# Optimization experiments

Measured on AMD Instinct MI355X. Metric: run time of the kernel, lower is better.

The kernel has to match this reference:

```python
import jax, jax.numpy as jnp
import numpy as np

N_E = 1024      # codes per sub-codebook
E_DIM = 64      # code dimension
BETA = 0.25     # commitment cost (VectorQuantizer(n_e, e_dim, 0.25))


def setup_inputs() -> dict:
    key = jax.random.key(0)
    k1, k2 = jax.random.split(key)
    bs, c, h, w = 16, 512, 32, 32
    m = c // E_DIM  # 8 sub-codebooks
    z = jax.random.normal(k1, (bs, c, h, w), dtype=jnp.float32)
    # taming-style init: uniform(-1/n_e, 1/n_e)
    codebooks = jax.random.uniform(
        k2, (m, N_E, E_DIM), dtype=jnp.float32,
        minval=-1.0 / N_E, maxval=1.0 / N_E)
    return {"z": z, "codebooks": codebooks}


def reference(z, codebooks):
    bs, c, h, w = z.shape
    m, n_e, e_dim = codebooks.shape
    N = bs * h * w
    # [bs,c,h,w] -> [bs,h,w,c] -> [m, N, e_dim]: batched over all m sub-codebooks at once
    zf = z.transpose(0, 2, 3, 1).reshape(N, m, e_dim).transpose(1, 0, 2)

    # squared L2 distances: ||z||^2 + ||e||^2 - 2 z.e   -> [m, N, n_e]
    d = ((zf ** 2).sum(-1, keepdims=True)
         + (codebooks ** 2).sum(-1)[:, None, :]
         - 2.0 * jnp.einsum('mnd,mkd->mnk', zf, codebooks))
    idx = jnp.argmin(d, axis=-1)  # [m, N]

    # gather nearest codes: [m, N, e_dim]
    zq = jnp.take_along_axis(codebooks, idx[:, :, None], axis=1)

    # per-sub-codebook VQ loss, summed over m (loss = sum(loss_list))
    codebook_loss = jnp.mean((jax.lax.stop_gradient(zq) - zf) ** 2, axis=(1, 2))
    commit_loss = jnp.mean((zq - jax.lax.stop_gradient(zf)) ** 2, axis=(1, 2))
    loss = jnp.sum(codebook_loss + BETA * commit_loss)

    # straight-through estimator
    zq_st = zf + jax.lax.stop_gradient(zq - zf)

    # reassemble: [m,N,d] -> [N,m*d] -> [bs,h,w,c] -> [bs,c,h,w]
    z_vq = zq_st.transpose(1, 0, 2).reshape(bs, h, w, c).transpose(0, 3, 1, 2)

    # concat of per-codebook index tensors along dim 0
    min_encoding_indices = idx.reshape(-1)  # [m*N]
    # per-code occupancy counts summed over the m codebooks -> [n_e]
    bin_count = jnp.zeros((n_e,), jnp.int32).at[min_encoding_indices].add(1)

    return z_vq, loss, min_encoding_indices, bin_count
```

## Files before the change

kernel.cpp:

```cpp
#include <hip/hip_runtime.h>
#include <cfloat>

#define BS 16
#define CC 512
#define HWD 1024
#define NN 16384
#define MM 8
#define NE 1024
#define ED 64

#define LOSS_OFF 8388608
#define IDX_OFF  8388609
#define BIN_OFF  8519681

#define TAU 4e-5f
#define UWIN 400u

#define WS_B     0
#define WS_IDX   32768
#define WS_CNT   557056
#define WS_LIST  557088
#define WS_OF    688160
#define WS_CAND  720928
#define WS_BMAT  3866656

typedef __attribute__((ext_vector_type(8))) short bf16x8;
typedef __attribute__((ext_vector_type(16))) float f32x16;

__device__ __forceinline__ unsigned short f2bf(float f) {
    unsigned int u = __float_as_uint(f);
    unsigned int r = (u + 0x7fffu + ((u >> 16) & 1u)) >> 16;
    return (unsigned short)r;
}
__device__ __forceinline__ float bf2f(unsigned short h) {
    return __uint_as_float(((unsigned int)h) << 16);
}
__device__ __forceinline__ unsigned umin_(unsigned a, unsigned b) { return a < b ? a : b; }
__device__ __forceinline__ unsigned umax_(unsigned a, unsigned b) { return a > b ? a : b; }
__device__ __forceinline__ unsigned umin3(unsigned a, unsigned b, unsigned c) {
    return umin_(umin_(a, b), c);
}

__device__ __forceinline__ float mul_rn(float a, float b) {
#pragma clang fp contract(off)
    return a * b;
}
__device__ __forceinline__ float add_rn(float a, float b) {
#pragma clang fp contract(off)
    return a + b;
}
__device__ __forceinline__ float sub_rn(float a, float b) {
#pragma clang fp contract(off)
    return a - b;
}

__device__ __forceinline__ float np_sumsq64(const float* x) {
    float r[8];
#pragma unroll
    for (int j = 0; j < 8; ++j) r[j] = mul_rn(x[j], x[j]);
#pragma unroll
    for (int i = 8; i < 64; i += 8) {
#pragma unroll
        for (int j = 0; j < 8; ++j) r[j] = add_rn(r[j], mul_rn(x[i + j], x[i + j]));
    }
    return add_rn(add_rn(add_rn(r[0], r[1]), add_rn(r[2], r[3])),
                  add_rn(add_rn(r[4], r[5]), add_rn(r[6], r[7])));
}

__device__ __forceinline__ float np_dot64(const float* zsh, const float4* cr4) {
    float v0 = 0.f, v1 = 0.f, v2 = 0.f, v3 = 0.f;
#pragma unroll
    for (int t = 0; t < 4; ++t) {
        float4 e0 = cr4[t * 4 + 0];
        float4 e1 = cr4[t * 4 + 1];
        float4 e2 = cr4[t * 4 + 2];
        float4 e3 = cr4[t * 4 + 3];
        const int d0 = 16 * t;
        v0 = add_rn(mul_rn(zsh[d0 + 0], e0.x),
             add_rn(mul_rn(zsh[d0 + 4], e1.x),
             add_rn(mul_rn(zsh[d0 + 8], e2.x),
             add_rn(mul_rn(zsh[d0 + 12], e3.x), v0))));
        v1 = add_rn(mul_rn(zsh[d0 + 1], e0.y),
             add_rn(mul_rn(zsh[d0 + 5], e1.y),
             add_rn(mul_rn(zsh[d0 + 9], e2.y),
             add_rn(mul_rn(zsh[d0 + 13], e3.y), v1))));
        v2 = add_rn(mul_rn(zsh[d0 + 2], e0.z),
             add_rn(mul_rn(zsh[d0 + 6], e1.z),
             add_rn(mul_rn(zsh[d0 + 10], e2.z),
             add_rn(mul_rn(zsh[d0 + 14], e3.z), v2))));
        v3 = add_rn(mul_rn(zsh[d0 + 3], e0.w),
             add_rn(mul_rn(zsh[d0 + 7], e1.w),
             add_rn(mul_rn(zsh[d0 + 11], e2.w),
             add_rn(mul_rn(zsh[d0 + 15], e3.w), v3))));
    }
    return add_rn(add_rn(v0, v1), add_rn(v2, v3));
}

__global__ __launch_bounds__(256) void prep_kernel(const float* __restrict__ cb,
                                                   float* __restrict__ Bhat,
                                                   uint4* __restrict__ Bmat,
                                                   float* __restrict__ out,
                                                   int* __restrict__ cnt) {
    const int tid = threadIdx.x;
    if (blockIdx.x < 32) {
        int i = blockIdx.x * 256 + tid;
        if (i == 0) { out[LOSS_OFF] = 0.0f; cnt[0] = 0; cnt[1] = 0; }
        if (i < NE) out[BIN_OFF + i] = 0.0f;
        const float4* r4 = (const float4*)(cb + (size_t)i * ED);
        float x[ED];
#pragma unroll
        for (int q = 0; q < 16; ++q) {
            float4 v = r4[q];
            x[q*4+0] = v.x; x[q*4+1] = v.y; x[q*4+2] = v.z; x[q*4+3] = v.w;
        }
        Bhat[i] = np_sumsq64(x);
        return;
    }
    int t = (blockIdx.x - 32) * 256 + tid;
    int lane = t & 63;
    int ct = (t >> 6) & 31;
    int rem = t >> 11;
    int c = rem % 9;
    int m = rem / 9;
    int h = lane >> 5;
    int k = ct * 32 + (lane & 31);

    unsigned short v[8];
#pragma unroll
    for (int j = 0; j < 8; ++j) v[j] = 0;

    if (c < 8) {
        int d0 = 16 * (c & 3) + 8 * h;
        const float* e = cb + ((size_t)m * NE + k) * ED + d0;
#pragma unroll
        for (int j = 0; j < 8; ++j) {
            float f = -2.0f * e[j];
            unsigned short hi = f2bf(f);
            v[j] = (c >= 4) ? f2bf(f - bf2f(hi)) : hi;
        }
    } else if (h == 0) {
        const float* e = cb + ((size_t)m * NE + k) * ED;
        float s = 0.f;
#pragma unroll
        for (int d = 0; d < ED; ++d) s += e[d] * e[d];
        v[0] = f2bf(s);
        v[1] = 0x3F80;
    }
    uint4 o;
    o.x = (unsigned)v[0] | ((unsigned)v[1] << 16);
    o.y = (unsigned)v[2] | ((unsigned)v[3] << 16);
    o.z = (unsigned)v[4] | ((unsigned)v[5] << 16);
    o.w = (unsigned)v[6] | ((unsigned)v[7] << 16);
    Bmat[t] = o;
}

__global__ __launch_bounds__(512, 4) void argmin_kernel(
        const float* __restrict__ z, const uint4* __restrict__ Bmat,
        int* __restrict__ idx_out, int* __restrict__ cnt,
        int* __restrict__ list, unsigned short* __restrict__ cand) {
    const int tid = threadIdx.x;
    const int m = blockIdx.y;
    const int row0 = blockIdx.x * 256;
    const int w = tid >> 6;
    const int l = tid & 63;
    const int h = l >> 5;
    const int r5 = l & 31;

    __shared__ uint4 ldsB[3][9 * 2 * 64];

    const int n_mine = row0 + w * 32 + r5;
    const int b = n_mine >> 10;
    const int hw = n_mine & (HWD - 1);
    const float* zbase = z + (((size_t)(b * CC + m * ED)) << 10) + hw;

    bf16x8 zh[4], zl[4];
#pragma unroll
    for (int i = 0; i < 4; ++i) {
        int o = 2 * i + h;
#pragma unroll
        for (int j = 0; j < 8; ++j) {
            float f = zbase[(size_t)(8 * o + j) << 10];
            unsigned short hb = f2bf(f);
            unsigned short lb = f2bf(f - bf2f(hb));
            zh[i][j] = (short)hb;
            zl[i][j] = (short)lb;
        }
    }
    bf16x8 ones12 = {0, 0, 0, 0, 0, 0, 0, 0};
    if (h == 0) { ones12[0] = (short)0x3F80; ones12[1] = (short)0x3F80; }

    unsigned rbm = 0xFFFFFFF0u, rsec = 0xFFFFFFFFu, rinfo = 0;
    int ccnt = 0;
    unsigned cq0 = 0, cq1 = 0, cq2 = 0;
    auto push = [&](unsigned id) {
        cq2 = (cq2 << 16) | (cq1 >> 16);
        cq1 = (cq1 << 16) | (cq0 >> 16);
        cq0 = (cq0 << 16) | (id & 0xFFFFu);
        ccnt++;
    };

    auto stage = [&](int g, int bufi) {
        for (int seg = w; seg < 18; seg += 8) {
            int c = seg >> 1, ct2 = seg & 1;
            const uint4* src = Bmat +
                ((size_t)((m * 9 + c) * 32 + (g * 2 + ct2)) << 6) + l;
            uint4* dst = &ldsB[bufi][(c * 2 + ct2) * 64];
            __builtin_amdgcn_global_load_lds(
                (const __attribute__((address_space(1))) unsigned int*)src,
                (__attribute__((address_space(3))) unsigned int*)dst, 16, 0, 0);
        }
    };

    auto process = [&](const f32x16& acc, unsigned tile) {
        unsigned u[16];
#pragma unroll
        for (int s = 0; s < 16; ++s)
            u[s] = (__float_as_uint(acc[s]) & 0xFFFFFFF0u) | (unsigned)s;
        unsigned b0 = umin_(u[0], u[1]),  s0 = umax_(u[0], u[1]);
        unsigned b1 = umin_(u[2], u[3]),  s1 = umax_(u[2], u[3]);
        unsigned b2 = umin_(u[4], u[5]),  s2 = umax_(u[4], u[5]);
        unsigned b3 = umin_(u[6], u[7]),  s3 = umax_(u[6], u[7]);
        unsigned b4 = umin_(u[8], u[9]),  s4 = umax_(u[8], u[9]);
        unsigned b5 = umin_(u[10], u[11]), s5 = umax_(u[10], u[11]);
        unsigned b6 = umin_(u[12], u[13]), s6 = umax_(u[12], u[13]);
        unsigned b7 = umin_(u[14], u[15]), s7 = umax_(u[14], u[15]);
        unsigned B0 = umin_(b0, b1), S0 = umin3(umax_(b0, b1), s0, s1);
        unsigned B1 = umin_(b2, b3), S1 = umin3(umax_(b2, b3), s2, s3);
        unsigned B2 = umin_(b4, b5), S2 = umin3(umax_(b4, b5), s4, s5);
        unsigned B3 = umin_(b6, b7), S3 = umin3(umax_(b6, b7), s6, s7);
        unsigned C0 = umin_(B0, B1), T0 = umin3(umax_(B0, B1), S0, S1);
        unsigned C1 = umin_(B2, B3), T1 = umin3(umax_(B2, B3), S2, S3);
        unsigned bt = umin_(C0, C1), st = umin3(umax_(C0, C1), T0, T1);

        unsigned oldrbm = rbm;
        bool take = bt < oldrbm;
        unsigned newrbm = take ? bt : oldrbm;
        unsigned limit = newrbm + UWIN;
        rsec = umin3(rsec, st, take ? oldrbm : bt);
        int sbt = (int)(bt & 15u);
        if (take) {
            if (bt + UWIN < oldrbm) ccnt = 0;
            push(tile * 32u + ((unsigned)sbt & 3u) +
                 8u * ((unsigned)sbt >> 2) + 4u * (unsigned)h);
            rinfo = (tile << 4) | (unsigned)sbt;
        }
        rbm = newrbm;
        unsigned gatev = take ? st : bt;
        if (gatev < limit) {
#pragma unroll
            for (int s = 0; s < 16; ++s) {
                if (u[s] < limit && !(take && s == sbt))
                    push(tile * 32u + ((unsigned)s & 3u) +
                         8u * ((unsigned)s >> 2) + 4u * (unsigned)h);
            }
        }
    };

    stage(0, 0);
    stage(1, 1);
    asm volatile("s_waitcnt vmcnt(2)" ::: "memory");
    __builtin_amdgcn_s_barrier();

    int bR = 0;
    for (int g = 0; g < 16; ++g) {
        int bW = bR + 2; if (bW >= 3) bW -= 3;
        if (g < 14) stage(g + 2, bW);
        const uint4* Bb = &ldsB[bR][0];

        f32x16 a0, a1;
#pragma unroll
        for (int s = 0; s < 16; ++s) { a0[s] = 0.0f; a1[s] = 0.0f; }
        bf16x8 sh0[4], sh1[4];
        __builtin_amdgcn_s_setprio(1);
#pragma unroll
        for (int c = 0; c < 4; ++c) {
            bf16x8 af0 = *(const bf16x8*)&Bb[(c * 2 + 0) * 64 + l];
            bf16x8 af1 = *(const bf16x8*)&Bb[(c * 2 + 1) * 64 + l];
            sh0[c] = af0; sh1[c] = af1;
            a0 = __builtin_amdgcn_mfma_f32_32x32x16_bf16(af0, zh[c], a0, 0, 0, 0);
            a1 = __builtin_amdgcn_mfma_f32_32x32x16_bf16(af1, zh[c], a1, 0, 0, 0);
        }
#pragma unroll
        for (int c = 4; c < 8; ++c) {
            bf16x8 af0 = *(const bf16x8*)&Bb[(c * 2 + 0) * 64 + l];
            bf16x8 af1 = *(const bf16x8*)&Bb[(c * 2 + 1) * 64 + l];
            a0 = __builtin_amdgcn_mfma_f32_32x32x16_bf16(af0, zh[c & 3], a0, 0, 0, 0);
            a1 = __builtin_amdgcn_mfma_f32_32x32x16_bf16(af1, zh[c & 3], a1, 0, 0, 0);
        }
#pragma unroll
        for (int c = 0; c < 4; ++c) {
            a0 = __builtin_amdgcn_mfma_f32_32x32x16_bf16(sh0[c], zl[c], a0, 0, 0, 0);
            a1 = __builtin_amdgcn_mfma_f32_32x32x16_bf16(sh1[c], zl[c], a1, 0, 0, 0);
        }
        {
            bf16x8 af0 = *(const bf16x8*)&Bb[(8 * 2 + 0) * 64 + l];
            bf16x8 af1 = *(const bf16x8*)&Bb[(8 * 2 + 1) * 64 + l];
            a0 = __builtin_amdgcn_mfma_f32_32x32x16_bf16(af0, ones12, a0, 0, 0, 0);
            a1 = __builtin_amdgcn_mfma_f32_32x32x16_bf16(af1, ones12, a1, 0, 0, 0);
        }
        __builtin_amdgcn_s_setprio(0);
        process(a0, (unsigned)(g * 2 + 0));
        process(a1, (unsigned)(g * 2 + 1));

        if (g < 14) {
            asm volatile("s_waitcnt vmcnt(2)" ::: "memory");
        } else if (g == 14) {
            asm volatile("s_waitcnt vmcnt(0)" ::: "memory");
        }
        if (g < 15) __builtin_amdgcn_s_barrier();
        bR = (bR == 2) ? 0 : bR + 1;
    }

    unsigned short* myslots = cand + ((size_t)(m * NN + n_mine) * 2 + h) * 6;
    if (ccnt) {
        unsigned* cp = (unsigned*)myslots;
        cp[0] = cq0; cp[1] = cq1; cp[2] = cq2;
    }

    int pcnt = __shfl_xor(ccnt, 32, 64);

    unsigned ss = rinfo & 15u, tile = rinfo >> 4;
    int k = (int)(tile * 32 + (ss & 3u) + 8u * (ss >> 2) + 4u * (unsigned)h);
    unsigned orbm = __shfl_xor(rbm, 32, 64);
    int ok = __shfl_xor(k, 32, 64);
    unsigned orsec = __shfl_xor(rsec, 32, 64);
    bool take = orbm < rbm;
    unsigned lose = take ? rbm : orbm;
    unsigned fb = take ? orbm : rbm;
    int fk = take ? ok : k;
    unsigned fs = umin3(rsec, orsec, lose);
    if (l < 32) {
        int mn = m * NN + n_mine;
        idx_out[mn] = fk;
        float margin = __uint_as_float(fs & 0xFFFFFFF0u) -
                       __uint_as_float(fb & 0xFFFFFFF0u);
        if (margin < TAU) {
            int p = atomicAdd(cnt, 1);
            if (p < 32768) {
                int c0 = ccnt > 6 ? 7 : ccnt;
                int c1 = pcnt > 6 ? 7 : pcnt;
                list[p] = mn | (c0 << 20) | (c1 << 24);
            }
        }
    }
}

__global__ __launch_bounds__(256) void cand_kernel(
        const float* __restrict__ z, const float* __restrict__ cb,
        const float* __restrict__ Bhat, int* __restrict__ cnt,
        const int* __restrict__ list, const unsigned short* __restrict__ cand,
        int* __restrict__ idx_out, int* __restrict__ oflist) {
    const int tid = threadIdx.x;
    const int lane = tid & 63;
    const int wv = tid >> 6;
    const int wid = (blockIdx.x * 256 + tid) >> 6;
    const int nw = gridDim.x * 4;
    const int total = cnt[0] < 32768 ? cnt[0] : 32768;

    __shared__ float zsh[4][ED];

    for (int r = wid; r < total; r += nw) {
        const int e = list[r];
        const int mn = e & 0xFFFFF;
        const int c0 = (e >> 20) & 15;
        const int c1 = (e >> 24) & 15;
        if (c0 == 7 || c1 == 7) {
            if (lane == 0) {
                int q = atomicAdd(cnt + 1, 1);
                if (q < 8192) oflist[q] = mn;
            }
            continue;
        }
        const int m = mn >> 14;
        const int n = mn & (NN - 1);
        const int b = n >> 10;
        const int hw = n & (HWD - 1);

        zsh[wv][lane] = z[(((size_t)(b * CC + m * ED + lane)) << 10) + hw];

        int kj = -1;
        if (lane < c0) kj = cand[(size_t)mn * 12 + lane];
        else if (lane >= 8 && lane < 8 + c1) kj = cand[(size_t)mn * 12 + 6 + (lane - 8)];

        float A = np_sumsq64(&zsh[wv][0]);

        float dref = FLT_MAX;
        if (kj >= 0) {
            const float4* cr4 = (const float4*)(cb + ((size_t)m * NE + kj) * ED);
            float C = np_dot64(&zsh[wv][0], cr4);
            dref = sub_rn(add_rn(A, Bhat[m * NE + kj]), mul_rn(2.0f, C));
        }
        int kk = (kj >= 0) ? kj : NE;
#pragma unroll
        for (int off = 32; off >= 1; off >>= 1) {
            float ov = __shfl_down(dref, off, 64);
            int oi = __shfl_down(kk, off, 64);
            if (ov < dref || (ov == dref && oi < kk)) { dref = ov; kk = oi; }
        }
        if (lane == 0) idx_out[mn] = kk;
    }
}

__global__ __launch_bounds__(256) void emul_kernel(
        const float* __restrict__ z, const float* __restrict__ cb,
        const float* __restrict__ Bhat, const int* __restrict__ cnt,
        const int* __restrict__ oflist, int* __restrict__ idx_out) {
    const int tid = threadIdx.x;
    const int lane = tid & 63;
    const int w = tid >> 6;
    const int total = cnt[1] < 8192 ? cnt[1] : 8192;

    __shared__ float zsh[ED];
    __shared__ float rbest[4];
    __shared__ int ridx[4];

    for (int r = blockIdx.x; r < total; r += gridDim.x) {
        const int mn = oflist[r];
        const int m = mn >> 14;
        const int n = mn & (NN - 1);
        const int b = n >> 10;
        const int hw = n & (HWD - 1);

        __syncthreads();
        if (tid < ED) {
            const float* zbase = z + (((size_t)(b * CC + m * ED)) << 10) + hw;
            zsh[tid] = zbase[(size_t)tid << 10];
        }
        __syncthreads();

        const float A = np_sumsq64(zsh);
        const float* cbm = cb + (size_t)m * NE * ED;
        const float* Bm = Bhat + m * NE;
        float best = FLT_MAX;
        int bidx = NE;
#pragma unroll
        for (int kk = 0; kk < 4; ++kk) {
            const int k = kk * 256 + tid;
            const float4* cr4 = (const float4*)(cbm + (size_t)k * ED);
            float C = np_dot64(zsh, cr4);
            float dk = sub_rn(add_rn(A, Bm[k]), mul_rn(2.0f, C));
            if (dk < best || (dk == best && k < bidx)) { best = dk; bidx = k; }
        }
#pragma unroll
        for (int off = 32; off >= 1; off >>= 1) {
            float ov = __shfl_down(best, off, 64);
            int oi = __shfl_down(bidx, off, 64);
            if (ov < best || (ov == best && oi < bidx)) { best = ov; bidx = oi; }
        }
        if (lane == 0) { rbest[w] = best; ridx[w] = bidx; }
        __syncthreads();
        if (tid == 0) {
            float bb = rbest[0]; int bi = ridx[0];
#pragma unroll
            for (int i = 1; i < 4; ++i) {
                if (rbest[i] < bb || (rbest[i] == bb && ridx[i] < bi)) {
                    bb = rbest[i]; bi = ridx[i];
                }
            }
            idx_out[mn] = bi;
        }
    }
}

__global__ __launch_bounds__(256) void output_kernel(
        const float* __restrict__ z, const float* __restrict__ cb,
        const int* __restrict__ idx_in, float* __restrict__ out) {
    const int tid = threadIdx.x;
    const int n = blockIdx.x * 256 + tid;
    const int m = blockIdx.y;
    const int b = n >> 10;
    const int hw = n & (HWD - 1);
    const int idx = idx_in[m * NN + n];

    out[IDX_OFF + m * NN + n] = (float)idx;

    const float* cr = cb + ((size_t)m * NE + (size_t)idx) * ED;
    const float* zbase = z + (((size_t)(b * CC + m * ED)) << 10) + hw;
    float* ob = out + (((size_t)(b * CC + m * ED)) << 10) + hw;

    double acc = 0.0;
#pragma unroll
    for (int d = 0; d < ED; ++d) {
        float c = cr[d];
        float zv = zbase[(size_t)d << 10];
        ob[(size_t)d << 10] = c;
        float diff = c - zv;
        acc += (double)diff * (double)diff;
    }

    __shared__ int hist[NE];
#pragma unroll
    for (int i = 0; i < 4; ++i) hist[tid + i * 256] = 0;
    __syncthreads();
    atomicAdd(&hist[idx], 1);

#pragma unroll
    for (int off = 32; off >= 1; off >>= 1)
        acc += __shfl_down(acc, off, 64);
    __shared__ double wsum[4];
    if ((tid & 63) == 0) wsum[tid >> 6] = acc;
    __syncthreads();
    if (tid == 0) {
        double t = wsum[0] + wsum[1] + wsum[2] + wsum[3];
        atomicAdd(out + LOSS_OFF, (float)(t * (1.25 / 1048576.0)));
    }
#pragma unroll
    for (int i = 0; i < 4; ++i) {
        int v = hist[tid + i * 256];
        if (v) atomicAdd(out + BIN_OFF + tid + i * 256, (float)v);
    }
}

extern "C" void kernel_launch(void* const* d_in, const int* in_sizes, int n_in,
                              void* d_out, int out_size, void* d_ws, size_t ws_size,
                              hipStream_t stream) {
    const float* z = (const float*)d_in[0];
    const float* cb = (const float*)d_in[1];
    float* out = (float*)d_out;
    char* ws = (char*)d_ws;
    float* Bhat = (float*)(ws + WS_B);
    int* idxw = (int*)(ws + WS_IDX);
    int* cnt = (int*)(ws + WS_CNT);
    int* list = (int*)(ws + WS_LIST);
    int* oflist = (int*)(ws + WS_OF);
    unsigned short* cand = (unsigned short*)(ws + WS_CAND);
    uint4* Bmat = (uint4*)(ws + WS_BMAT);

    prep_kernel<<<dim3(608), dim3(256), 0, stream>>>(cb, Bhat, Bmat, out, cnt);
    argmin_kernel<<<dim3(NN / 256, MM), dim3(512), 0, stream>>>(
        z, Bmat, idxw, cnt, list, cand);
    cand_kernel<<<dim3(256), dim3(256), 0, stream>>>(
        z, cb, Bhat, cnt, list, cand, idxw, oflist);
    emul_kernel<<<dim3(256), dim3(256), 0, stream>>>(
        z, cb, Bhat, cnt, oflist, idxw);
    output_kernel<<<dim3(NN / 256, MM), dim3(256), 0, stream>>>(z, cb, idxw, out);
}
```

Before: 174.1 us.

## Fuse candidate re-check and fallback argmin into output kernel via packed flags

The argmin kernel now packs the ambiguity flag and candidate counts into the index word instead of appending to a global atomic list. The output kernel collects flagged rows per block in shared memory and re-resolves them before writing outputs, using the cand path or a full wave-level scan of all 1024 codes on overflow. This removes two kernel launches, the global atomic counters and the list indirection. The cost is that fallback work now runs inside output blocks and can create per-block imbalance.

```diff
diff --git a/kernel.cpp b/kernel.cpp
--- a/kernel.cpp
+++ b/kernel.cpp
@@ -18,9 +18,6 @@
 
 #define WS_B     0
 #define WS_IDX   32768
-#define WS_CNT   557056
-#define WS_LIST  557088
-#define WS_OF    688160
 #define WS_CAND  720928
 #define WS_BMAT  3866656
 
@@ -99,12 +96,11 @@
 __global__ __launch_bounds__(256) void prep_kernel(const float* __restrict__ cb,
                                                    float* __restrict__ Bhat,
                                                    uint4* __restrict__ Bmat,
-                                                   float* __restrict__ out,
-                                                   int* __restrict__ cnt) {
+                                                   float* __restrict__ out) {
     const int tid = threadIdx.x;
     if (blockIdx.x < 32) {
         int i = blockIdx.x * 256 + tid;
-        if (i == 0) { out[LOSS_OFF] = 0.0f; cnt[0] = 0; cnt[1] = 0; }
+        if (i == 0) out[LOSS_OFF] = 0.0f;
         if (i < NE) out[BIN_OFF + i] = 0.0f;
         const float4* r4 = (const float4*)(cb + (size_t)i * ED);
         float x[ED];
@@ -156,8 +152,7 @@
 
 __global__ __launch_bounds__(512, 4) void argmin_kernel(
         const float* __restrict__ z, const uint4* __restrict__ Bmat,
-        int* __restrict__ idx_out, int* __restrict__ cnt,
-        int* __restrict__ list, unsigned short* __restrict__ cand) {
+        int* __restrict__ idx_out, unsigned short* __restrict__ cand) {
     const int tid = threadIdx.x;
     const int m = blockIdx.y;
     const int row0 = blockIdx.x * 256;
@@ -331,146 +326,110 @@
     unsigned fs = umin3(rsec, orsec, lose);
     if (l < 32) {
         int mn = m * NN + n_mine;
-        idx_out[mn] = fk;
+        int pack = fk;
         float margin = __uint_as_float(fs & 0xFFFFFFF0u) -
                        __uint_as_float(fb & 0xFFFFFFF0u);
         if (margin < TAU) {
-            int p = atomicAdd(cnt, 1);
-            if (p < 32768) {
-                int c0 = ccnt > 6 ? 7 : ccnt;
-                int c1 = pcnt > 6 ? 7 : pcnt;
-                list[p] = mn | (c0 << 20) | (c1 << 24);
-            }
-        }
-    }
-}
-
-__global__ __launch_bounds__(256) void cand_kernel(
+            int c0 = ccnt > 6 ? 7 : ccnt;
+            int c1 = pcnt > 6 ? 7 : pcnt;
+            pack |= (1 << 30) | (c0 << 16) | (c1 << 20);
+        }
+        idx_out[mn] = pack;
+    }
+}
+
+__global__ __launch_bounds__(256) void output_kernel(
         const float* __restrict__ z, const float* __restrict__ cb,
-        const float* __restrict__ Bhat, int* __restrict__ cnt,
-        const int* __restrict__ list, const unsigned short* __restrict__ cand,
-        int* __restrict__ idx_out, int* __restrict__ oflist) {
+        const float* __restrict__ Bhat, const unsigned short* __restrict__ cand,
+        const int* __restrict__ idx_in, float* __restrict__ out) {
     const int tid = threadIdx.x;
     const int lane = tid & 63;
     const int wv = tid >> 6;
-    const int wid = (blockIdx.x * 256 + tid) >> 6;
-    const int nw = gridDim.x * 4;
-    const int total = cnt[0] < 32768 ? cnt[0] : 32768;
-
-    __shared__ float zsh[4][ED];
-
-    for (int r = wid; r < total; r += nw) {
-        const int e = list[r];
-        const int mn = e & 0xFFFFF;
-        const int c0 = (e >> 20) & 15;
-        const int c1 = (e >> 24) & 15;
-        if (c0 == 7 || c1 == 7) {
-            if (lane == 0) {
-                int q = atomicAdd(cnt + 1, 1);
-                if (q < 8192) oflist[q] = mn;
-            }
-            continue;
-        }
-        const int m = mn >> 14;
-        const int n = mn & (NN - 1);
-        const int b = n >> 10;
-        const int hw = n & (HWD - 1);
-
-        zsh[wv][lane] = z[(((size_t)(b * CC + m * ED + lane)) << 10) + hw];
-
-        int kj = -1;
-        if (lane < c0) kj = cand[(size_t)mn * 12 + lane];
-        else if (lane >= 8 && lane < 8 + c1) kj = cand[(size_t)mn * 12 + 6 + (lane - 8)];
-
-        float A = np_sumsq64(&zsh[wv][0]);
-
-        float dref = FLT_MAX;
-        if (kj >= 0) {
-            const float4* cr4 = (const float4*)(cb + ((size_t)m * NE + kj) * ED);
-            float C = np_dot64(&zsh[wv][0], cr4);
-            dref = sub_rn(add_rn(A, Bhat[m * NE + kj]), mul_rn(2.0f, C));
-        }
-        int kk = (kj >= 0) ? kj : NE;
-#pragma unroll
-        for (int off = 32; off >= 1; off >>= 1) {
-            float ov = __shfl_down(dref, off, 64);
-            int oi = __shfl_down(kk, off, 64);
-            if (ov < dref || (ov == dref && oi < kk)) { dref = ov; kk = oi; }
-        }
-        if (lane == 0) idx_out[mn] = kk;
-    }
-}
-
-__global__ __launch_bounds__(256) void emul_kernel(
-        const float* __restrict__ z, const float* __restrict__ cb,
-        const float* __restrict__ Bhat, const int* __restrict__ cnt,
-        const int* __restrict__ oflist, int* __restrict__ idx_out) {
-    const int tid = threadIdx.x;
-    const int lane = tid & 63;
-    const int w = tid >> 6;
-    const int total = cnt[1] < 8192 ? cnt[1] : 8192;
-
-    __shared__ float zsh[ED];
-    __shared__ float rbest[4];
-    __shared__ int ridx[4];
-
-    for (int r = blockIdx.x; r < total; r += gridDim.x) {
-        const int mn = oflist[r];
-        const int m = mn >> 14;
-        const int n = mn & (NN - 1);
-        const int b = n >> 10;
-        const int hw = n & (HWD - 1);
-
-        __syncthreads();
-        if (tid < ED) {
-            const float* zbase = z + (((size_t)(b * CC + m * ED)) << 10) + hw;
-            zsh[tid] = zbase[(size_t)tid << 10];
-        }
-        __syncthreads();
-
-        const float A = np_sumsq64(zsh);
-        const float* cbm = cb + (size_t)m * NE * ED;
-        const float* Bm = Bhat + m * NE;
-        float best = FLT_MAX;
-        int bidx = NE;
-#pragma unroll
-        for (int kk = 0; kk < 4; ++kk) {
-            const int k = kk * 256 + tid;
-            const float4* cr4 = (const float4*)(cbm + (size_t)k * ED);
-            float C = np_dot64(zsh, cr4);
-            float dk = sub_rn(add_rn(A, Bm[k]), mul_rn(2.0f, C));
-            if (dk < best || (dk == best && k < bidx)) { best = dk; bidx = k; }
-        }
-#pragma unroll
-        for (int off = 32; off >= 1; off >>= 1) {
-            float ov = __shfl_down(best, off, 64);
-            int oi = __shfl_down(bidx, off, 64);
-            if (ov < best || (ov == best && oi < bidx)) { best = ov; bidx = oi; }
-        }
-        if (lane == 0) { rbest[w] = best; ridx[w] = bidx; }
-        __syncthreads();
-        if (tid == 0) {
-            float bb = rbest[0]; int bi = ridx[0];
-#pragma unroll
-            for (int i = 1; i < 4; ++i) {
-                if (rbest[i] < bb || (rbest[i] == bb && ridx[i] < bi)) {
-                    bb = rbest[i]; bi = ridx[i];
-                }
-            }
-            idx_out[mn] = bi;
-        }
-    }
-}
-
-__global__ __launch_bounds__(256) void output_kernel(
-        const float* __restrict__ z, const float* __restrict__ cb,
-        const int* __restrict__ idx_in, float* __restrict__ out) {
-    const int tid = threadIdx.x;
     const int n = blockIdx.x * 256 + tid;
     const int m = blockIdx.y;
+    const int row0 = blockIdx.x * 256;
+
+    __shared__ int hist[NE];
+    __shared__ int ridx[256];
+    __shared__ int pks[256];
+    __shared__ short flist[256];
+    __shared__ int fcnt;
+    __shared__ float zsh[4][ED];
+
+    if (tid == 0) fcnt = 0;
+#pragma unroll
+    for (int i = 0; i < 4; ++i) hist[tid + i * 256] = 0;
+    const int pk = idx_in[m * NN + n];
+    pks[tid] = pk;
+    ridx[tid] = pk & 1023;
+    __syncthreads();
+    if (pk & (1 << 30)) {
+        int q = atomicAdd(&fcnt, 1);
+        flist[q] = (short)tid;
+    }
+    __syncthreads();
+
+    const int fc = fcnt;
+    for (int r = wv; r < fc; r += 4) {
+        const int t = flist[r];
+        const int rn = row0 + t;
+        const int rb = rn >> 10;
+        const int rhw = rn & (HWD - 1);
+        const int mn = m * NN + rn;
+        const int c0 = (pks[t] >> 16) & 15;
+        const int c1 = (pks[t] >> 20) & 15;
+
+        zsh[wv][lane] = z[(((size_t)(rb * CC + m * ED + lane)) << 10) + rhw];
+        float A = np_sumsq64(&zsh[wv][0]);
+
+        int kk;
+        if (c0 == 7 || c1 == 7) {
+            const float* cbm = cb + (size_t)m * NE * ED;
+            const float* Bm = Bhat + m * NE;
+            float best = FLT_MAX;
+            int bidx = NE;
+            for (int i = 0; i < 16; ++i) {
+                const int k = i * 64 + lane;
+                const float4* cr4 = (const float4*)(cbm + (size_t)k * ED);
+                float C = np_dot64(&zsh[wv][0], cr4);
+                float dk = sub_rn(add_rn(A, Bm[k]), mul_rn(2.0f, C));
+                if (dk < best || (dk == best && k < bidx)) { best = dk; bidx = k; }
+            }
+#pragma unroll
+            for (int off = 32; off >= 1; off >>= 1) {
+                float ov = __shfl_down(best, off, 64);
+                int oi = __shfl_down(bidx, off, 64);
+                if (ov < best || (ov == best && oi < bidx)) { best = ov; bidx = oi; }
+            }
+            kk = bidx;
+        } else {
+            int kj = -1;
+            if (lane < c0) kj = cand[(size_t)mn * 12 + lane];
+            else if (lane >= 8 && lane < 8 + c1)
+                kj = cand[(size_t)mn * 12 + 6 + (lane - 8)];
+
+            float dref = FLT_MAX;
+            if (kj >= 0) {
+                const float4* cr4 = (const float4*)(cb + ((size_t)m * NE + kj) * ED);
+                float C = np_dot64(&zsh[wv][0], cr4);
+                dref = sub_rn(add_rn(A, Bhat[m * NE + kj]), mul_rn(2.0f, C));
+            }
+            int ki = (kj >= 0) ? kj : NE;
+#pragma unroll
+            for (int off = 32; off >= 1; off >>= 1) {
+                float ov = __shfl_down(dref, off, 64);
+                int oi = __shfl_down(ki, off, 64);
+                if (ov < dref || (ov == dref && oi < ki)) { dref = ov; ki = oi; }
+            }
+            kk = ki;
+        }
+        if (lane == 0) ridx[t] = kk;
+    }
+    __syncthreads();
+
     const int b = n >> 10;
     const int hw = n & (HWD - 1);
-    const int idx = idx_in[m * NN + n];
+    const int idx = ridx[tid];
 
     out[IDX_OFF + m * NN + n] = (float)idx;
 
@@ -488,10 +447,6 @@
         acc += (double)diff * (double)diff;
     }
 
-    __shared__ int hist[NE];
-#pragma unroll
-    for (int i = 0; i < 4; ++i) hist[tid + i * 256] = 0;
-    __syncthreads();
     atomicAdd(&hist[idx], 1);
 
 #pragma unroll
@@ -504,6 +459,7 @@
         double t = wsum[0] + wsum[1] + wsum[2] + wsum[3];
         atomicAdd(out + LOSS_OFF, (float)(t * (1.25 / 1048576.0)));
     }
+    __syncthreads();
 #pragma unroll
     for (int i = 0; i < 4; ++i) {
         int v = hist[tid + i * 256];
@@ -520,18 +476,12 @@
     char* ws = (char*)d_ws;
     float* Bhat = (float*)(ws + WS_B);
     int* idxw = (int*)(ws + WS_IDX);
-    int* cnt = (int*)(ws + WS_CNT);
-    int* list = (int*)(ws + WS_LIST);
-    int* oflist = (int*)(ws + WS_OF);
     unsigned short* cand = (unsigned short*)(ws + WS_CAND);
     uint4* Bmat = (uint4*)(ws + WS_BMAT);
 
-    prep_kernel<<<dim3(608), dim3(256), 0, stream>>>(cb, Bhat, Bmat, out, cnt);
+    prep_kernel<<<dim3(608), dim3(256), 0, stream>>>(cb, Bhat, Bmat, out);
     argmin_kernel<<<dim3(NN / 256, MM), dim3(512), 0, stream>>>(
-        z, Bmat, idxw, cnt, list, cand);
-    cand_kernel<<<dim3(256), dim3(256), 0, stream>>>(
-        z, cb, Bhat, cnt, list, cand, idxw, oflist);
-    emul_kernel<<<dim3(256), dim3(256), 0, stream>>>(
-        z, cb, Bhat, cnt, oflist, idxw);
-    output_kernel<<<dim3(NN / 256, MM), dim3(256), 0, stream>>>(z, cb, idxw, out);
-}
+        z, Bmat, idxw, cand);
+    output_kernel<<<dim3(NN / 256, MM), dim3(256), 0, stream>>>(
+        z, cb, Bhat, cand, idxw, out);
+}
```

Measured after the change: 159.8 us. 8.3% less time.
